# Optimization experiments

Measured on AMD Instinct MI355X. Metric: run time of the kernel, lower is better.

## Reference

```python
import jax, jax.numpy as jnp
import numpy as np

B, N, E, K, H = 4, 2048, 512, 16, 8
EMB = 2 * E  # MultiheadAttention embed_dim = input_enc * 2


def setup_inputs() -> dict:
    key = jax.random.key(0)
    ks = jax.random.split(key, 6)
    s = 0.02
    return {
        "x": jax.random.normal(ks[0], (B, N, E), jnp.float32),
        "x_enc": jax.random.normal(ks[1], (B, N, EMB), jnp.float32),
        "w_in": jax.random.normal(ks[2], (3 * EMB, EMB), jnp.float32) * s,
        "b_in": jnp.zeros((3 * EMB,), jnp.float32),
        "w_out": jax.random.normal(ks[3], (EMB, EMB), jnp.float32) * s,
        "b_out": jnp.zeros((EMB,), jnp.float32),
        "k": K,
    }


def _knn_mean(x, k):
    # x: (B, N, E). torch code transposes to (B, E, N) and treats the E channel
    # rows as the 'points' for kNN (distance matrix is (B, E, E)).
    xt = jnp.swapaxes(x, 1, 2)                      # (B, E, N)
    sq = jnp.sum(xt * xt, axis=-1)                  # (B, E)
    dist = sq[:, :, None] + sq[:, None, :] - 2.0 * jnp.einsum("ben,bfn->bef", xt, xt)
    idx = jax.lax.top_k(-dist, k)[1]                # (B, E, k) smallest distances
    # fused gather + mean: avoid the (B, E, E, N) expand from the torch code
    nbrs = jnp.take_along_axis(xt[:, None, :, :], idx[:, :, :, None], axis=2)  # (B, E, k, N)
    return jnp.swapaxes(jnp.mean(nbrs, axis=2), 1, 2)  # (B, N, E)


def _mha(q, kv, w_in, b_in, w_out, b_out, h):
    # faithful torch nn.MultiheadAttention (batch_first) forward
    wq, wk, wv = jnp.split(w_in, 3, axis=0)
    bq, bk, bv = jnp.split(b_in, 3, axis=0)
    Q = q @ wq.T + bq
    Kt = kv @ wk.T + bk
    V = kv @ wv.T + bv
    b, l, emb = Q.shape
    m = Kt.shape[1]
    d = emb // h

    def split_heads(t):
        return t.reshape(t.shape[0], t.shape[1], h, d).transpose(0, 2, 1, 3)

    Qh, Kh, Vh = split_heads(Q), split_heads(Kt), split_heads(V)
    scores = jnp.einsum("bhld,bhmd->bhlm", Qh, Kh) / jnp.sqrt(jnp.float32(d))
    att = jax.nn.softmax(scores, axis=-1)
    o = jnp.einsum("bhlm,bhmd->bhld", att, Vh)      # (B, H, L, d)
    o = o.transpose(0, 2, 1, 3).reshape(b, l, emb)
    return o @ w_out.T + b_out


def reference(x, x_enc, w_in, b_in, w_out, b_out, k):
    b, n, e = x.shape
    x_knn = _knn_mean(x, k)                          # (B, N, E)
    cat = jnp.concatenate([jnp.swapaxes(x, 1, 2), jnp.swapaxes(x_knn, 1, 2)], axis=-1)  # (B, E, 2N)
    # faithful to torch .view(-1, 2*E, N): row-interleaving reshape, NOT a transpose
    q = jnp.swapaxes(cat.reshape(b, 2 * e, n), 1, 2)  # (B, N, 2E)
    attn = _mha(q, x_enc, w_in, b_in, w_out, b_out, H)  # (B, N, 2E)
    return jnp.concatenate([q, attn], axis=1)         # (B, 2N, 2E)
```

## Files before the change

kernel.cpp:

```cpp
#include <hip/hip_runtime.h>
#include <hip/hip_bf16.h>

#define B_ 4
#define N_ 2048
#define E_ 512
#define EMB_ 1024
#define H_ 8
#define D_ 128
#define KNN_ 16

typedef short short8_t __attribute__((ext_vector_type(8)));
typedef short short4_t __attribute__((ext_vector_type(4)));
typedef float float4_t __attribute__((ext_vector_type(4)));

__device__ __forceinline__ short f2bf(float f) {
  unsigned u = __float_as_uint(f);
  unsigned r = u + 0x7fffu + ((u >> 16) & 1u);
  return (short)(r >> 16);
}

__device__ __forceinline__ unsigned pk2bf(float a, float b) {
  float2 f; f.x = a; f.y = b;
  __hip_bfloat162 h = __float22bfloat162_rn(f);
  return *(unsigned*)&h;
}

__device__ __forceinline__ float fexp2(float x) {
  return __builtin_amdgcn_exp2f(x);
}

__global__ __launch_bounds__(256) void k_sqnp_part(const float* __restrict__ x,
                                                   float* __restrict__ part) {
  const int t = blockIdx.x * 256 + threadIdx.x;
  if (t >= B_ * E_ * 16) return;
  const int be = t & (B_ * E_ - 1), blk = t >> 11;
  const int b = be >> 9, e = be & (E_ - 1);
  const float* p = x + (size_t)b * N_ * E_ + (size_t)blk * 128 * E_ + e;
  float lane[16];
#pragma unroll
  for (int l = 0; l < 16; l++) {
    float pr[8];
#pragma unroll
    for (int j = 0; j < 8; j++) {
      float v = p[(size_t)(j * 16 + l) * E_];
      pr[j] = __fmul_rn(v, v);
    }
    float s01 = __fadd_rn(pr[0], pr[1]);
    float s23 = __fadd_rn(pr[2], pr[3]);
    float s45 = __fadd_rn(pr[4], pr[5]);
    float s67 = __fadd_rn(pr[6], pr[7]);
    lane[l] = __fadd_rn(__fadd_rn(s01, s23), __fadd_rn(s45, s67));
  }
  float bb[8];
#pragma unroll
  for (int l = 0; l < 8; l++) bb[l] = __fadd_rn(lane[l], lane[l + 8]);
  float cc[4];
#pragma unroll
  for (int l = 0; l < 4; l++) cc[l] = __fadd_rn(bb[l], bb[l + 4]);
  part[(size_t)be * 16 + blk] =
      __fadd_rn(__fadd_rn(cc[0], cc[1]), __fadd_rn(cc[2], cc[3]));
}

__global__ __launch_bounds__(256) void k_sqnp_fin(const float* __restrict__ part,
                                                  float* __restrict__ sq) {
  const int t = blockIdx.x * 256 + threadIdx.x;
  if (t >= B_ * E_) return;
  const float* bs = part + (size_t)t * 16;
  float t1[8], t2[4];
#pragma unroll
  for (int l = 0; l < 8; l++) t1[l] = __fadd_rn(bs[2 * l], bs[2 * l + 1]);
#pragma unroll
  for (int l = 0; l < 4; l++) t2[l] = __fadd_rn(t1[2 * l], t1[2 * l + 1]);
  sq[t] = __fadd_rn(__fadd_rn(t2[0], t2[1]), __fadd_rn(t2[2], t2[3]));
}

__global__ __launch_bounds__(256) void k_gram_sym(const float* __restrict__ x,
                                                  float* __restrict__ g) {
  __shared__ float xs[32][36];
  __shared__ float ys[32][36];
  int p = blockIdx.x;
  const int b = blockIdx.y;
  int ti = 0;
  while (p >= 16 - ti) { p -= 16 - ti; ti++; }
  const int tj = ti + p;
  const int i0 = ti * 32, j0 = tj * 32;
  const int tid = threadIdx.x;
  const int li = tid & 15, lj = tid >> 4;
  const int snn = tid >> 3, sc4 = (tid & 7) * 4;
  const float* xb = x + (size_t)b * N_ * E_;

  float a00 = 0.f, a01 = 0.f, a10 = 0.f, a11 = 0.f;
  float4 px = *(const float4*)(xb + (size_t)snn * E_ + i0 + sc4);
  float4 py = *(const float4*)(xb + (size_t)snn * E_ + j0 + sc4);

  for (int n0 = 0; n0 < N_; n0 += 32) {
    __syncthreads();
    *(float4*)&xs[snn][sc4] = px;
    *(float4*)&ys[snn][sc4] = py;
    __syncthreads();
    if (n0 + 32 < N_) {
      px = *(const float4*)(xb + (size_t)(n0 + 32 + snn) * E_ + i0 + sc4);
      py = *(const float4*)(xb + (size_t)(n0 + 32 + snn) * E_ + j0 + sc4);
    }
#pragma unroll
    for (int nn = 0; nn < 32; nn++) {
      const float2 va = *(const float2*)&xs[nn][li * 2];
      const float2 vb = *(const float2*)&ys[nn][lj * 2];
      a00 = __fadd_rn(a00, __fmul_rn(va.x, vb.x));
      a01 = __fadd_rn(a01, __fmul_rn(va.x, vb.y));
      a10 = __fadd_rn(a10, __fmul_rn(va.y, vb.x));
      a11 = __fadd_rn(a11, __fmul_rn(va.y, vb.y));
    }
  }
  float* gb = g + (size_t)b * E_ * E_;
  const int i = i0 + li * 2, j = j0 + lj * 2;
  gb[(size_t)i * E_ + j]           = a00;
  gb[(size_t)i * E_ + j + 1]       = a01;
  gb[(size_t)(i + 1) * E_ + j]     = a10;
  gb[(size_t)(i + 1) * E_ + j + 1] = a11;
  if (ti != tj) {
    gb[(size_t)j * E_ + i]           = a00;
    gb[(size_t)(j + 1) * E_ + i]     = a01;
    gb[(size_t)j * E_ + i + 1]       = a10;
    gb[(size_t)(j + 1) * E_ + i + 1] = a11;
  }
}

__global__ __launch_bounds__(256) void k_topk(const float* __restrict__ sq,
                                              const float* __restrict__ g,
                                              int* __restrict__ idxout) {
  const int bi = blockIdx.x;
  const int b = bi >> 9, i = bi & (E_ - 1);
  const int tid = threadIdx.x;
  const float* gb = g + ((size_t)b * E_ + i) * E_;
  const float* sqb = sq + ((size_t)b << 9);
  __shared__ float val[E_];
  __shared__ float rv[256];
  __shared__ int ri[256];
  const float sqi = sqb[i];
  for (int j = tid; j < E_; j += 256) {
    val[j] = __fsub_rn(__fadd_rn(sqi, sqb[j]), __fmul_rn(2.0f, gb[j]));
  }
  __syncthreads();
  for (int t = 0; t < KNN_; t++) {
    float best = 3.0e38f; int bidx = E_;
    for (int j = tid; j < E_; j += 256) {
      float v = val[j];
      if (v < best) { best = v; bidx = j; }
    }
    rv[tid] = best; ri[tid] = bidx;
    __syncthreads();
    for (int s = 128; s > 0; s >>= 1) {
      if (tid < s) {
        float v2 = rv[tid + s]; int i2 = ri[tid + s];
        if (v2 < rv[tid] || (v2 == rv[tid] && i2 < ri[tid])) {
          rv[tid] = v2; ri[tid] = i2;
        }
      }
      __syncthreads();
    }
    if (tid == 0) {
      idxout[(size_t)bi * KNN_ + t] = ri[0];
      val[ri[0]] = 3.0e38f;
    }
    __syncthreads();
  }
}

__global__ __launch_bounds__(256) void k_knnmean(const float* __restrict__ x,
                                                 const int* __restrict__ idx,
                                                 float* __restrict__ out) {
  const int n = blockIdx.x, b = blockIdx.y;
  const int tid = threadIdx.x;
  __shared__ float xrow[E_];
  const float* xr = x + ((size_t)b * N_ + n) * E_;
  for (int i = tid; i < E_; i += 256) xrow[i] = xr[i];
  __syncthreads();
  float* orow = out + ((size_t)b * (2 * N_) + n) * EMB_;
  for (int i = tid; i < E_; i += 256) {
    const int* id = idx + ((size_t)b * E_ + i) * KNN_;
    float s = 0.f;
#pragma unroll
    for (int t = 0; t < KNN_; t++) s = __fadd_rn(s, xrow[id[t]]);
    float2 w; w.x = xrow[i]; w.y = s * (1.0f / 16.0f);
    *(float2*)&orow[2 * i] = w;
  }
}

__global__ __launch_bounds__(256) void k_cvt(const float* __restrict__ src,
                                             short* __restrict__ dst, int n8) {
  const int t = blockIdx.x * 256 + threadIdx.x;
  if (t >= n8) return;
  const float* s = src + (size_t)t * 8;
  float4 a = *(const float4*)s, b = *(const float4*)(s + 4);
  short8_t v;
  v[0] = f2bf(a.x); v[1] = f2bf(a.y); v[2] = f2bf(a.z); v[3] = f2bf(a.w);
  v[4] = f2bf(b.x); v[5] = f2bf(b.y); v[6] = f2bf(b.z); v[7] = f2bf(b.w);
  *(short8_t*)(dst + (size_t)t * 8) = v;
}

__global__ __launch_bounds__(256) void k_cvt_q(const float* __restrict__ outq,
                                               short* __restrict__ dst) {
  const int t = blockIdx.x * 256 + threadIdx.x;
  const int row = t >> 7, c = (t & 127) * 8;
  const int b = row >> 11, n = row & (N_ - 1);
  const float* s = outq + ((size_t)b * 2 * N_ + n) * EMB_ + c;
  float4 a = *(const float4*)s, bb = *(const float4*)(s + 4);
  short8_t v;
  v[0] = f2bf(a.x);  v[1] = f2bf(a.y);  v[2] = f2bf(a.z);  v[3] = f2bf(a.w);
  v[4] = f2bf(bb.x); v[5] = f2bf(bb.y); v[6] = f2bf(bb.z); v[7] = f2bf(bb.w);
  *(short8_t*)(dst + (size_t)row * EMB_ + c) = v;
}

template<int MODE>
__global__ __launch_bounds__(256) void k_gemm_bf16(
    const short* __restrict__ X, const short* __restrict__ W,
    const float* __restrict__ bias, short* __restrict__ Yb,
    float* __restrict__ Yf) {
  __shared__ __align__(16) short As[128 * 64];
  __shared__ __align__(16) short Bs[128 * 64];
  const int tid = threadIdx.x;
  const int row0 = blockIdx.x * 128, col0 = blockIdx.y * 128;
  const int l = tid & 63, lg = l >> 4, lq = l & 15;
  const int w = tid >> 6, wm = w >> 1, wn = w & 1;
  float4_t acc[4][4];
#pragma unroll
  for (int i = 0; i < 4; i++)
#pragma unroll
    for (int j = 0; j < 4; j++) {
      acc[i][j][0] = 0.f; acc[i][j][1] = 0.f; acc[i][j][2] = 0.f; acc[i][j][3] = 0.f;
    }

  int rr_[4], cc_[4];
#pragma unroll
  for (int ii = 0; ii < 4; ii++) {
    const int cid = ii * 256 + tid;
    rr_[ii] = cid >> 3; cc_[ii] = cid & 7;
  }
  short8_t ar[4], br[4];
#pragma unroll
  for (int ii = 0; ii < 4; ii++) {
    ar[ii] = *(const short8_t*)(X + (size_t)(row0 + rr_[ii]) * EMB_ + cc_[ii] * 8);
    br[ii] = *(const short8_t*)(W + (size_t)(col0 + rr_[ii]) * EMB_ + cc_[ii] * 8);
  }

  for (int kt = 0; kt < 16; kt++) {
    __syncthreads();
#pragma unroll
    for (int ii = 0; ii < 4; ii++) {
      const int idx = rr_[ii] * 64 + ((cc_[ii] * 8) ^ ((rr_[ii] & 7) << 3));
      *(short8_t*)&As[idx] = ar[ii];
      *(short8_t*)&Bs[idx] = br[ii];
    }
    __syncthreads();
    if (kt < 15) {
#pragma unroll
      for (int ii = 0; ii < 4; ii++) {
        ar[ii] = *(const short8_t*)(X + (size_t)(row0 + rr_[ii]) * EMB_ + (kt + 1) * 64 + cc_[ii] * 8);
        br[ii] = *(const short8_t*)(W + (size_t)(col0 + rr_[ii]) * EMB_ + (kt + 1) * 64 + cc_[ii] * 8);
      }
    }
#pragma unroll
    for (int kk = 0; kk < 2; kk++) {
      short8_t af[4], bf[4];
#pragma unroll
      for (int mi = 0; mi < 4; mi++) {
        const int r = wm * 64 + mi * 16 + lq;
        af[mi] = *(const short8_t*)&As[r * 64 + ((kk * 32 + lg * 8) ^ ((r & 7) << 3))];
      }
#pragma unroll
      for (int ni = 0; ni < 4; ni++) {
        const int r = wn * 64 + ni * 16 + lq;
        bf[ni] = *(const short8_t*)&Bs[r * 64 + ((kk * 32 + lg * 8) ^ ((r & 7) << 3))];
      }
#pragma unroll
      for (int mi = 0; mi < 4; mi++)
#pragma unroll
        for (int ni = 0; ni < 4; ni++)
          acc[mi][ni] = __builtin_amdgcn_mfma_f32_16x16x32_bf16(af[mi], bf[ni], acc[mi][ni], 0, 0, 0);
    }
  }
#pragma unroll
  for (int ni = 0; ni < 4; ni++) {
    const int col = col0 + wn * 64 + ni * 16 + lq;
    const float bv = bias[col];
#pragma unroll
    for (int mi = 0; mi < 4; mi++) {
#pragma unroll
      for (int j = 0; j < 4; j++) {
        const int m = row0 + wm * 64 + mi * 16 + lg * 4 + j;
        const float v = acc[mi][ni][j] + bv;
        if (MODE == 0) {
          Yb[(size_t)m * EMB_ + col] = f2bf(v);
        } else if (MODE == 1) {
          const int b2 = m >> 11, n2 = m & (N_ - 1);
          Yf[((size_t)b2 * 2 * N_ + N_ + n2) * EMB_ + col] = v;
        } else {
          const int b2 = m >> 11, n2 = m & (N_ - 1);
          Yb[((size_t)b2 * EMB_ + col) * N_ + n2] = f2bf(v);
        }
      }
    }
  }
}

__global__ __launch_bounds__(256, 4) void k_flash_bf16(
    const short* __restrict__ Qg, const short* __restrict__ Kg,
    const short* __restrict__ Vtg, short* __restrict__ Og) {
  __shared__ __align__(16) short Ks[64 * 128];
  __shared__ __align__(16) short Vs[128 * 64];
  __shared__ __align__(16) short Ps[4][16 * 64];
  const int tid = threadIdx.x;
  const int w = tid >> 6, l = tid & 63, lg = l >> 4, lq = l & 15;
  const int bid = blockIdx.x;
  const int bh = (bid & 7) * 4 + ((bid >> 3) >> 5);
  const int rt = (bid >> 3) & 31;
  const int b = bh >> 3, h = bh & 7;
  const float c1 = 0.08838834764831845f * 1.4426950408889634f;
  const size_t bhoff = (size_t)b * N_ * EMB_ + (size_t)h * D_;
  const int qsw = (lq & 7) << 3;

  int koff[4], vofs[4], klds[4], vlds[4];
#pragma unroll
  for (int ii = 0; ii < 4; ii++) {
    const int cid = ii * 256 + tid;
    const int kr = cid >> 4, kc = cid & 15;
    const int vr = cid >> 3, vc = cid & 7;
    koff[ii] = kr * EMB_ + kc * 8;
    vofs[ii] = vr * N_ + vc * 8;
    klds[ii] = kr * 128 + ((kc * 8) ^ ((kr & 7) << 3));
    vlds[ii] = vr * 64 + ((vc * 8) ^ ((vr & 7) << 3));
  }
  const short* Kt0 = Kg + bhoff;
  const short* Vt0 = Vtg + (size_t)b * EMB_ * N_ + (size_t)(h * D_) * N_;

  short8_t qf[4];
  {
    const short* qrow = Qg + bhoff + (size_t)(rt * 64 + w * 16 + lq) * EMB_;
#pragma unroll
    for (int kk = 0; kk < 4; kk++)
      qf[kk] = *(const short8_t*)(qrow + kk * 32 + lg * 8);
  }
  float4_t oacc[8];
#pragma unroll
  for (int mc = 0; mc < 8; mc++) {
    oacc[mc][0] = 0.f; oacc[mc][1] = 0.f; oacc[mc][2] = 0.f; oacc[mc][3] = 0.f;
  }
  float m = -3.0e38f, lsum = 0.f;

  short8_t kreg[4], vreg[4];
#pragma unroll
  for (int ii = 0; ii < 4; ii++) {
    kreg[ii] = *(const short8_t*)(Kt0 + koff[ii]);
    vreg[ii] = *(const short8_t*)(Vt0 + vofs[ii]);
  }
#pragma unroll
  for (int ii = 0; ii < 4; ii++) {
    *(short8_t*)&Ks[klds[ii]] = kreg[ii];
    *(short8_t*)&Vs[vlds[ii]] = vreg[ii];
  }
  __syncthreads();

  for (int kt = 0; kt < N_ / 64; kt++) {
    if (kt + 1 < N_ / 64) {
      const short* Kt = Kt0 + (size_t)((kt + 1) * 64) * EMB_;
      const short* Vt = Vt0 + (kt + 1) * 64;
#pragma unroll
      for (int ii = 0; ii < 4; ii++) {
        kreg[ii] = *(const short8_t*)(Kt + koff[ii]);
        vreg[ii] = *(const short8_t*)(Vt + vofs[ii]);
      }
    }

    float4_t sc[4];
    __builtin_amdgcn_s_setprio(1);
#pragma unroll
    for (int c = 0; c < 4; c++) {
      sc[c][0] = 0.f; sc[c][1] = 0.f; sc[c][2] = 0.f; sc[c][3] = 0.f;
      const int krow = c * 16 + lq;
#pragma unroll
      for (int kk = 0; kk < 4; kk++) {
        short8_t kf = *(const short8_t*)&Ks[krow * 128 + ((kk * 32 + lg * 8) ^ qsw)];
        sc[c] = __builtin_amdgcn_mfma_f32_16x16x32_bf16(kf, qf[kk], sc[c], 0, 0, 0);
      }
    }
    __builtin_amdgcn_s_setprio(0);

    float tm = sc[0][0];
#pragma unroll
    for (int c = 0; c < 4; c++) {
      tm = fmaxf(tm, fmaxf(fmaxf(sc[c][0], sc[c][1]), fmaxf(sc[c][2], sc[c][3])));
    }
    tm = fmaxf(tm, __shfl_xor(tm, 16));
    tm = fmaxf(tm, __shfl_xor(tm, 32));
    if (__any(tm > m + 62.7f)) {
      const float mn = fmaxf(m, tm);
      const float alpha = fexp2((m - mn) * c1);
      m = mn;
      lsum *= alpha;
#pragma unroll
      for (int mc = 0; mc < 8; mc++) {
        oacc[mc][0] *= alpha; oacc[mc][1] *= alpha;
        oacc[mc][2] *= alpha; oacc[mc][3] *= alpha;
      }
    }
    const float mc1 = m * c1;
    float ps = 0.f;
#pragma unroll
    for (int c = 0; c < 4; c++) {
      float p0 = fexp2(__builtin_fmaf(sc[c][0], c1, -mc1));
      float p1 = fexp2(__builtin_fmaf(sc[c][1], c1, -mc1));
      float p2 = fexp2(__builtin_fmaf(sc[c][2], c1, -mc1));
      float p3 = fexp2(__builtin_fmaf(sc[c][3], c1, -mc1));
      ps += (p0 + p1) + (p2 + p3);
      uint2 pw; pw.x = pk2bf(p0, p1); pw.y = pk2bf(p2, p3);
      *(uint2*)&Ps[w][lq * 64 + ((c * 16 + lg * 4) ^ qsw)] = pw;
    }
    ps += __shfl_xor(ps, 16);
    ps += __shfl_xor(ps, 32);
    lsum += ps;

    __builtin_amdgcn_s_setprio(1);
#pragma unroll
    for (int kk = 0; kk < 2; kk++) {
      short8_t pf = *(const short8_t*)&Ps[w][lq * 64 + ((kk * 32 + lg * 8) ^ qsw)];
#pragma unroll
      for (int mc = 0; mc < 8; mc++) {
        const int dd = mc * 16 + lq;
        short8_t vf = *(const short8_t*)&Vs[dd * 64 + ((kk * 32 + lg * 8) ^ qsw)];
        oacc[mc] = __builtin_amdgcn_mfma_f32_16x16x32_bf16(vf, pf, oacc[mc], 0, 0, 0);
      }
    }
    __builtin_amdgcn_s_setprio(0);

    __syncthreads();
    if (kt + 1 < N_ / 64) {
#pragma unroll
      for (int ii = 0; ii < 4; ii++) {
        *(short8_t*)&Ks[klds[ii]] = kreg[ii];
        *(short8_t*)&Vs[vlds[ii]] = vreg[ii];
      }
      __syncthreads();
    }
  }

  const float linv = 1.0f / lsum;
  short* orow = Og + bhoff + (size_t)(rt * 64 + w * 16 + lq) * EMB_;
#pragma unroll
  for (int mc = 0; mc < 8; mc++) {
    short4_t o;
    o[0] = f2bf(oacc[mc][0] * linv); o[1] = f2bf(oacc[mc][1] * linv);
    o[2] = f2bf(oacc[mc][2] * linv); o[3] = f2bf(oacc[mc][3] * linv);
    *(short4_t*)&orow[mc * 16 + lg * 4] = o;
  }
}

extern "C" void kernel_launch(void* const* d_in, const int* in_sizes, int n_in,
                              void* d_out, int out_size, void* d_ws, size_t ws_size,
                              hipStream_t stream) {
  const float* x     = (const float*)d_in[0];
  const float* x_enc = (const float*)d_in[1];
  const float* w_in  = (const float*)d_in[2];
  const float* b_in  = (const float*)d_in[3];
  const float* w_out = (const float*)d_in[4];
  const float* b_out = (const float*)d_in[5];
  float* out = (float*)d_out;
  char* wsb = (char*)d_ws;

  const size_t oG    = 0;
  const size_t oSq   = oG + (size_t)B_ * E_ * E_ * 4;
  const size_t oPart = oSq + (size_t)B_ * E_ * 4;
  const size_t oIdx  = oPart + (size_t)B_ * E_ * 16 * 4;
  const size_t oXq   = (oIdx + (size_t)B_ * E_ * KNN_ * 4 + 255) & ~(size_t)255;
  const size_t sB    = (size_t)B_ * N_ * EMB_ * 2;
  const size_t oXe   = oXq + sB;
  const size_t oWin  = oXe + sB;
  const size_t oWo   = oWin + 3ull * EMB_ * EMB_ * 2;
  const size_t oQ    = oWo + (size_t)EMB_ * EMB_ * 2;
  const size_t oK    = oQ + sB;
  const size_t oV    = oK + sB;
  const size_t oO    = oV + sB;
  const size_t need  = oO + sB;

  float* g    = (float*)(wsb + oG);
  float* sqv  = (float*)(wsb + oSq);
  float* part = (float*)(wsb + oPart);
  int*   idx  = (int*)(wsb + oIdx);
  short* Xq   = (short*)(wsb + oXq);
  short* Xe   = (short*)(wsb + oXe);
  short* Win  = (short*)(wsb + oWin);
  short* Wo   = (short*)(wsb + oWo);
  short* Qb   = (short*)(wsb + oQ);
  short* Kb   = (short*)(wsb + oK);
  short* Vb   = (short*)(wsb + oV);
  short* Ob   = (ws_size >= need) ? (short*)(wsb + oO) : Qb;

  k_sqnp_part<<<dim3(B_ * E_ * 16 / 256), 256, 0, stream>>>(x, part);
  k_sqnp_fin<<<dim3(B_ * E_ / 256), 256, 0, stream>>>(part, sqv);
  k_gram_sym<<<dim3(136, B_), 256, 0, stream>>>(x, g);
  k_topk<<<dim3(B_ * E_), 256, 0, stream>>>(sqv, g, idx);
  k_knnmean<<<dim3(N_, B_), 256, 0, stream>>>(x, idx, out);

  k_cvt<<<dim3(4096), 256, 0, stream>>>(x_enc, Xe, B_ * N_ * EMB_ / 8);
  k_cvt<<<dim3(1536), 256, 0, stream>>>(w_in, Win, 3 * EMB_ * EMB_ / 8);
  k_cvt<<<dim3(512), 256, 0, stream>>>(w_out, Wo, EMB_ * EMB_ / 8);
  k_cvt_q<<<dim3(4096), 256, 0, stream>>>(out, Xq);

  k_gemm_bf16<0><<<dim3(64, 8), 256, 0, stream>>>(Xq, Win, b_in, Qb, nullptr);
  k_gemm_bf16<0><<<dim3(64, 8), 256, 0, stream>>>(Xe, Win + (size_t)EMB_ * EMB_,
                                                  b_in + EMB_, Kb, nullptr);
  k_gemm_bf16<2><<<dim3(64, 8), 256, 0, stream>>>(Xe, Win + 2ull * EMB_ * EMB_,
                                                  b_in + 2 * EMB_, Vb, nullptr);

  k_flash_bf16<<<dim3(1024), 256, 0, stream>>>(Qb, Kb, Vb, Ob);

  k_gemm_bf16<1><<<dim3(64, 8), 256, 0, stream>>>(Ob, Wo, b_out, nullptr, out);
}
```

Measured before the change: 395.3 us.

## Switch flash attention to 32x32x16 MFMA with 32 query rows per wave

Rewrites the flash-attention kernel so each wave handles 32 query rows using 32x32x16 bf16 MFMA instructions instead of 16 rows with 16x16x32. Each block now covers 128 query rows, which halves the grid and halves the number of times each K/V tile is loaded and staged per query. The P scratch buffer and the output layout change to match the 32x32 accumulator layout. This raises register pressure, so launch bounds drop to 2 blocks per CU, which lowers occupancy and may hurt latency hiding.

New measurement: 354.8 us. 10.3% less time.

```diff
diff --git a/kernel.cpp b/kernel.cpp
--- a/kernel.cpp
+++ b/kernel.cpp
@@ -12,6 +12,7 @@
 typedef short short8_t __attribute__((ext_vector_type(8)));
 typedef short short4_t __attribute__((ext_vector_type(4)));
 typedef float float4_t __attribute__((ext_vector_type(4)));
+typedef float float16_t __attribute__((ext_vector_type(16)));
 
 __device__ __forceinline__ short f2bf(float f) {
   unsigned u = __float_as_uint(f);
@@ -304,21 +305,22 @@
   }
 }
 
-__global__ __launch_bounds__(256, 4) void k_flash_bf16(
+__global__ __launch_bounds__(256, 2) void k_flash_bf16(
     const short* __restrict__ Qg, const short* __restrict__ Kg,
     const short* __restrict__ Vtg, short* __restrict__ Og) {
   __shared__ __align__(16) short Ks[64 * 128];
   __shared__ __align__(16) short Vs[128 * 64];
-  __shared__ __align__(16) short Ps[4][16 * 64];
+  __shared__ __align__(16) short Ps[4][32 * 64];
   const int tid = threadIdx.x;
-  const int w = tid >> 6, l = tid & 63, lg = l >> 4, lq = l & 15;
+  const int w = tid >> 6, l = tid & 63;
+  const int hi = l >> 5, l5 = l & 31;
   const int bid = blockIdx.x;
-  const int bh = (bid & 7) * 4 + ((bid >> 3) >> 5);
-  const int rt = (bid >> 3) & 31;
+  const int bh = (bid & 7) * 4 + ((bid >> 3) >> 4);
+  const int rt = (bid >> 3) & 15;
   const int b = bh >> 3, h = bh & 7;
   const float c1 = 0.08838834764831845f * 1.4426950408889634f;
   const size_t bhoff = (size_t)b * N_ * EMB_ + (size_t)h * D_;
-  const int qsw = (lq & 7) << 3;
+  const int psw = (l5 & 7) << 3;
 
   int koff[4], vofs[4], klds[4], vlds[4];
 #pragma unroll
@@ -334,18 +336,18 @@
   const short* Kt0 = Kg + bhoff;
   const short* Vt0 = Vtg + (size_t)b * EMB_ * N_ + (size_t)(h * D_) * N_;
 
-  short8_t qf[4];
+  short8_t qf[8];
   {
-    const short* qrow = Qg + bhoff + (size_t)(rt * 64 + w * 16 + lq) * EMB_;
-#pragma unroll
-    for (int kk = 0; kk < 4; kk++)
-      qf[kk] = *(const short8_t*)(qrow + kk * 32 + lg * 8);
-  }
-  float4_t oacc[8];
-#pragma unroll
-  for (int mc = 0; mc < 8; mc++) {
-    oacc[mc][0] = 0.f; oacc[mc][1] = 0.f; oacc[mc][2] = 0.f; oacc[mc][3] = 0.f;
-  }
+    const short* qrow = Qg + bhoff + (size_t)(rt * 128 + w * 32 + l5) * EMB_;
+#pragma unroll
+    for (int s = 0; s < 8; s++)
+      qf[s] = *(const short8_t*)(qrow + s * 16 + hi * 8);
+  }
+  float16_t oacc[4];
+#pragma unroll
+  for (int dg = 0; dg < 4; dg++)
+#pragma unroll
+    for (int r = 0; r < 16; r++) oacc[dg][r] = 0.f;
   float m = -3.0e38f, lsum = 0.f;
 
   short8_t kreg[4], vreg[4];
@@ -372,26 +374,25 @@
       }
     }
 
-    float4_t sc[4];
+    float16_t s0, s1;
+#pragma unroll
+    for (int r = 0; r < 16; r++) { s0[r] = 0.f; s1[r] = 0.f; }
     __builtin_amdgcn_s_setprio(1);
 #pragma unroll
-    for (int c = 0; c < 4; c++) {
-      sc[c][0] = 0.f; sc[c][1] = 0.f; sc[c][2] = 0.f; sc[c][3] = 0.f;
-      const int krow = c * 16 + lq;
-#pragma unroll
-      for (int kk = 0; kk < 4; kk++) {
-        short8_t kf = *(const short8_t*)&Ks[krow * 128 + ((kk * 32 + lg * 8) ^ qsw)];
-        sc[c] = __builtin_amdgcn_mfma_f32_16x16x32_bf16(kf, qf[kk], sc[c], 0, 0, 0);
-      }
+    for (int s = 0; s < 8; s++) {
+      const int col = (s * 16 + hi * 8) ^ psw;
+      short8_t kf0 = *(const short8_t*)&Ks[l5 * 128 + col];
+      short8_t kf1 = *(const short8_t*)&Ks[(32 + l5) * 128 + col];
+      s0 = __builtin_amdgcn_mfma_f32_32x32x16_bf16(kf0, qf[s], s0, 0, 0, 0);
+      s1 = __builtin_amdgcn_mfma_f32_32x32x16_bf16(kf1, qf[s], s1, 0, 0, 0);
     }
     __builtin_amdgcn_s_setprio(0);
 
-    float tm = sc[0][0];
-#pragma unroll
-    for (int c = 0; c < 4; c++) {
-      tm = fmaxf(tm, fmaxf(fmaxf(sc[c][0], sc[c][1]), fmaxf(sc[c][2], sc[c][3])));
-    }
-    tm = fmaxf(tm, __shfl_xor(tm, 16));
+    float tm = s0[0];
+#pragma unroll
+    for (int r = 1; r < 16; r++) tm = fmaxf(tm, s0[r]);
+#pragma unroll
+    for (int r = 0; r < 16; r++) tm = fmaxf(tm, s1[r]);
     tm = fmaxf(tm, __shfl_xor(tm, 32));
     if (__any(tm > m + 62.7f)) {
       const float mn = fmaxf(m, tm);
@@ -399,36 +400,44 @@
       m = mn;
       lsum *= alpha;
 #pragma unroll
-      for (int mc = 0; mc < 8; mc++) {
-        oacc[mc][0] *= alpha; oacc[mc][1] *= alpha;
-        oacc[mc][2] *= alpha; oacc[mc][3] *= alpha;
-      }
+      for (int dg = 0; dg < 4; dg++)
+#pragma unroll
+        for (int r = 0; r < 16; r++) oacc[dg][r] *= alpha;
     }
     const float mc1 = m * c1;
     float ps = 0.f;
 #pragma unroll
-    for (int c = 0; c < 4; c++) {
-      float p0 = fexp2(__builtin_fmaf(sc[c][0], c1, -mc1));
-      float p1 = fexp2(__builtin_fmaf(sc[c][1], c1, -mc1));
-      float p2 = fexp2(__builtin_fmaf(sc[c][2], c1, -mc1));
-      float p3 = fexp2(__builtin_fmaf(sc[c][3], c1, -mc1));
+    for (int g = 0; g < 4; g++) {
+      float p0 = fexp2(__builtin_fmaf(s0[4 * g + 0], c1, -mc1));
+      float p1 = fexp2(__builtin_fmaf(s0[4 * g + 1], c1, -mc1));
+      float p2 = fexp2(__builtin_fmaf(s0[4 * g + 2], c1, -mc1));
+      float p3 = fexp2(__builtin_fmaf(s0[4 * g + 3], c1, -mc1));
       ps += (p0 + p1) + (p2 + p3);
       uint2 pw; pw.x = pk2bf(p0, p1); pw.y = pk2bf(p2, p3);
-      *(uint2*)&Ps[w][lq * 64 + ((c * 16 + lg * 4) ^ qsw)] = pw;
-    }
-    ps += __shfl_xor(ps, 16);
+      *(uint2*)&Ps[w][l5 * 64 + ((g * 8 + hi * 4) ^ psw)] = pw;
+    }
+#pragma unroll
+    for (int g = 0; g < 4; g++) {
+      float p0 = fexp2(__builtin_fmaf(s1[4 * g + 0], c1, -mc1));
+      float p1 = fexp2(__builtin_fmaf(s1[4 * g + 1], c1, -mc1));
+      float p2 = fexp2(__builtin_fmaf(s1[4 * g + 2], c1, -mc1));
+      float p3 = fexp2(__builtin_fmaf(s1[4 * g + 3], c1, -mc1));
+      ps += (p0 + p1) + (p2 + p3);
+      uint2 pw; pw.x = pk2bf(p0, p1); pw.y = pk2bf(p2, p3);
+      *(uint2*)&Ps[w][l5 * 64 + ((32 + g * 8 + hi * 4) ^ psw)] = pw;
+    }
     ps += __shfl_xor(ps, 32);
     lsum += ps;
 
     __builtin_amdgcn_s_setprio(1);
 #pragma unroll
-    for (int kk = 0; kk < 2; kk++) {
-      short8_t pf = *(const short8_t*)&Ps[w][lq * 64 + ((kk * 32 + lg * 8) ^ qsw)];
-#pragma unroll
-      for (int mc = 0; mc < 8; mc++) {
-        const int dd = mc * 16 + lq;
-        short8_t vf = *(const short8_t*)&Vs[dd * 64 + ((kk * 32 + lg * 8) ^ qsw)];
-        oacc[mc] = __builtin_amdgcn_mfma_f32_16x16x32_bf16(vf, pf, oacc[mc], 0, 0, 0);
+    for (int ks = 0; ks < 4; ks++) {
+      const int col = (ks * 16 + hi * 8) ^ psw;
+      short8_t pf = *(const short8_t*)&Ps[w][l5 * 64 + col];
+#pragma unroll
+      for (int dg = 0; dg < 4; dg++) {
+        short8_t vf = *(const short8_t*)&Vs[(dg * 32 + l5) * 64 + col];
+        oacc[dg] = __builtin_amdgcn_mfma_f32_32x32x16_bf16(vf, pf, oacc[dg], 0, 0, 0);
       }
     }
     __builtin_amdgcn_s_setprio(0);
@@ -445,13 +454,18 @@
   }
 
   const float linv = 1.0f / lsum;
-  short* orow = Og + bhoff + (size_t)(rt * 64 + w * 16 + lq) * EMB_;
-#pragma unroll
-  for (int mc = 0; mc < 8; mc++) {
-    short4_t o;
-    o[0] = f2bf(oacc[mc][0] * linv); o[1] = f2bf(oacc[mc][1] * linv);
-    o[2] = f2bf(oacc[mc][2] * linv); o[3] = f2bf(oacc[mc][3] * linv);
-    *(short4_t*)&orow[mc * 16 + lg * 4] = o;
+  short* orow = Og + bhoff + (size_t)(rt * 128 + w * 32 + l5) * EMB_;
+#pragma unroll
+  for (int dg = 0; dg < 4; dg++) {
+#pragma unroll
+    for (int g = 0; g < 4; g++) {
+      float p0 = oacc[dg][4 * g + 0] * linv;
+      float p1 = oacc[dg][4 * g + 1] * linv;
+      float p2 = oacc[dg][4 * g + 2] * linv;
+      float p3 = oacc[dg][4 * g + 3] * linv;
+      uint2 ow; ow.x = pk2bf(p0, p1); ow.y = pk2bf(p2, p3);
+      *(uint2*)&orow[dg * 32 + g * 8 + hi * 4] = ow;
+    }
   }
 }
 
@@ -512,7 +526,7 @@
   k_gemm_bf16<2><<<dim3(64, 8), 256, 0, stream>>>(Xe, Win + 2ull * EMB_ * EMB_,
                                                   b_in + 2 * EMB_, Vb, nullptr);
 
-  k_flash_bf16<<<dim3(1024), 256, 0, stream>>>(Qb, Kb, Vb, Ob);
+  k_flash_bf16<<<dim3(512), 256, 0, stream>>>(Qb, Kb, Vb, Ob);
 
   k_gemm_bf16<1><<<dim3(64, 8), 256, 0, stream>>>(Ob, Wo, b_out, nullptr, out);
 }
```
